# Performance work log

Measured on AMD Instinct MI355X. Metric: run time of the kernel, lower is better.

## Reference

```python
import jax, jax.numpy as jnp
import numpy as np

N_GROUPS = 4


def setup_inputs() -> dict:
    key = jax.random.key(0)
    ks = jax.random.split(key, 6)
    I, J, B = 512, 512, 4  # query tokens, key tokens, grid batch (B = 1 * n_groups)
    n_dim, out_per_group = 128, 4  # n_heads // n_groups = 16 // 4
    grid_q = jax.random.normal(ks[0], (I, 3), dtype=jnp.float32)
    grid_kv = jax.random.normal(ks[1], (B, J, 3), dtype=jnp.float32)
    W1 = jax.random.normal(ks[2], (3, n_dim), dtype=jnp.float32) * (1.0 / np.sqrt(3))
    b1 = jnp.zeros((n_dim,), dtype=jnp.float32)
    W2 = jax.random.normal(ks[3], (n_dim, n_dim), dtype=jnp.float32) * (1.0 / np.sqrt(n_dim))
    b2 = jnp.zeros((n_dim,), dtype=jnp.float32)
    W3 = jax.random.normal(ks[4], (n_dim, out_per_group), dtype=jnp.float32) * (1.0 / np.sqrt(n_dim))
    b3 = jnp.zeros((out_per_group,), dtype=jnp.float32)
    return {"grid_q": grid_q, "grid_kv": grid_kv, "W1": W1, "b1": b1,
            "W2": W2, "b2": b2, "W3": W3, "b3": b3}


def reference(grid_q, grid_kv, W1, b1, W2, b2, W3, b3):
    # grid_q: [I, 3] -> [1, I, 3]; grid_kv: [B, J, 3]
    gq = grid_q[None, :, :]
    # pairwise position difference: [B, I, J, 3]
    pos = gq[:, :, None, :] - grid_kv[:, None, :, :]
    # sign-log transform
    bias = jnp.sign(pos) * jnp.log1p(jnp.abs(pos))
    # tiny MLP: 3 -> n_dim -> n_dim -> heads//groups, pointwise over (B, I, J)
    h = jax.nn.relu(jnp.einsum('bijc,cd->bijd', bias, W1) + b1)
    h = jax.nn.relu(jnp.einsum('bijd,de->bije', h, W2) + b2)
    out = jnp.einsum('bije,eo->bijo', h, W3) + b3  # [B, I, J, O]
    # rearrange '(b g) i j o -> b (g o) i j' with g = N_GROUPS
    B, I, J, O = out.shape
    out = out.reshape(B // N_GROUPS, N_GROUPS, I, J, O)
    out = jnp.transpose(out, (0, 1, 4, 2, 3)).reshape(B // N_GROUPS, N_GROUPS * O, I, J)
    return out
```

## Files before the change

### kernel.cpp

```cpp
#include <hip/hip_runtime.h>
#include <math.h>

#define NDIM 128
#define TILE 64
#define NBLOCKS 2048
#define POS_PER_BLOCK 512
#define ITERS 8
#define CH 512

typedef __attribute__((ext_vector_type(8)))  short  short8;
typedef __attribute__((ext_vector_type(4)))  float  float4v;
typedef __attribute__((ext_vector_type(16))) float  float16;

__device__ __forceinline__ unsigned cvt_pk(float lo, float hi) {
    unsigned r;
    asm("v_cvt_pk_bf16_f32 %0, %1, %2" : "=v"(r) : "v"(lo), "v"(hi));
    return r;
}

__device__ __forceinline__ int kmap(int c, int jj) {
    return 32 * (c >> 2) + 16 * ((c >> 1) & 1) + 4 * (c & 1) + ((jj >> 2) << 3) + (jj & 3);
}

__global__ __launch_bounds__(256, 3)
void crpb_mfma4(const float* __restrict__ gq,
                const float* __restrict__ gkv,
                const float* __restrict__ W1,
                const float* __restrict__ b1,
                const float* __restrict__ W2,
                const float* __restrict__ b2,
                const float* __restrict__ W3,
                const float* __restrict__ b3,
                float* __restrict__ out)
{
    __shared__ __align__(16) unsigned short ash[16 * CH];
    __shared__ __align__(16) unsigned short h2s[16 * CH];
    __shared__ __align__(16) float b2s[NDIM];

    const int tid   = threadIdx.x;
    const int lane  = tid & 63;
    const int w     = __builtin_amdgcn_readfirstlane(tid >> 6);
    const int l31   = lane & 31;
    const int lhalf = lane >> 5;
    const int m16   = lane & 15;
    const int q16   = lane >> 4;

    if (tid < NDIM) b2s[tid] = b2[tid];

    const int ct = w;

    short8 a2f[8];
    #pragma unroll
    for (int ks = 0; ks < 8; ++ks) {
        const int c = 2 * ks + lhalf;
        unsigned t0[4];
        #pragma unroll
        for (int t = 0; t < 4; ++t) {
            const int d0 = kmap(c, 2 * t), d1 = d0 + 1;
            const int e0 = ct * 32 + l31;
            t0[t] = cvt_pk(W2[d0 * 128 + e0], W2[d1 * 128 + e0]);
        }
        __builtin_memcpy(&a2f[ks], t0, 16);
    }

    short8 w3t[4];
    #pragma unroll
    for (int ks = 0; ks < 4; ++ks) {
        const int c = ks * 4 + q16;
        unsigned tt[4];
        #pragma unroll
        for (int t = 0; t < 4; ++t) {
            const int k0 = kmap(c, 2 * t), k1 = k0 + 1;
            const float lo = (m16 < 4) ? W3[k0 * 4 + m16] : 0.0f;
            const float hi = (m16 < 4) ? W3[k1 * 4 + m16] : 0.0f;
            tt[t] = cvt_pk(lo, hi);
        }
        __builtin_memcpy(&w3t[ks], tt, 16);
    }
    float b3v[4];
    #pragma unroll
    for (int r = 0; r < 4; ++r) b3v[r] = (q16 == 0) ? b3[r] : 0.0f;

    __syncthreads();

    const int posblock = blockIdx.x * POS_PER_BLOCK;
    const int bb = posblock >> 18;
    const int i  = (posblock >> 9) & 511;
    const float q0 = gq[i * 3 + 0], q1 = gq[i * 3 + 1], q2 = gq[i * 3 + 2];

    unsigned short* aw        = ash + 4 * w * CH + lane * 8;
    const unsigned short* br  = ash + lhalf * CH + l31 * 8;
    unsigned short* cw        = h2s + (4 * ct + lhalf) * CH + l31 * 8;
    const unsigned short* dr  = h2s + q16 * CH + (w * 16 + m16) * 8;

    const float* kvp0 = gkv + (size_t)((bb << 9) + lane) * 3;
    float* obase = out + (((size_t)bb) << 20) + ((size_t)i << 9) + w * 16 + m16;

    float kv0 = kvp0[0], kv1 = kvp0[1], kv2 = kvp0[2];

    for (int it = 0; it < ITERS; ++it) {
        const int jb = it * TILE;

        {
            const float d0 = q0 - kv0, d1 = q1 - kv1, d2 = q2 - kv2;
            const float* kvn = kvp0 + ((it + 1) & 7) * (TILE * 3);
            kv0 = kvn[0]; kv1 = kvn[1]; kv2 = kvn[2];

            const float f0 = copysignf(__logf(1.0f + fabsf(d0)), d0);
            const float f1 = copysignf(__logf(1.0f + fabsf(d1)), d1);
            const float f2 = copysignf(__logf(1.0f + fabsf(d2)), d2);
            #pragma unroll
            for (int u = 0; u < 4; ++u) {
                const int c = 4 * w + u;
                unsigned pk[4];
                #pragma unroll
                for (int t = 0; t < 4; ++t) {
                    const int ch0 = kmap(c, 2 * t), ch1 = ch0 + 1;
                    float h0 = fmaf(f2, W1[256 + ch0], fmaf(f1, W1[128 + ch0],
                               fmaf(f0, W1[ch0], b1[ch0])));
                    float h1 = fmaf(f2, W1[256 + ch1], fmaf(f1, W1[128 + ch1],
                               fmaf(f0, W1[ch1], b1[ch1])));
                    pk[t] = cvt_pk(fmaxf(h0, 0.0f), fmaxf(h1, 0.0f));
                }
                short8 v; __builtin_memcpy(&v, pk, 16);
                *(short8*)(aw + u * CH) = v;
            }
        }
        __syncthreads();

        float16 acc0, acc1;
        #pragma unroll
        for (int qr = 0; qr < 4; ++qr) {
            float4v i0 = *(const float4v*)&b2s[ct * 32 + 8 * qr + 4 * lhalf];
            #pragma unroll
            for (int t = 0; t < 4; ++t) { acc0[4 * qr + t] = i0[t]; acc1[4 * qr + t] = i0[t]; }
        }
        #pragma unroll
        for (int ks = 0; ks < 8; ++ks) {
            short8 bf0 = *(const short8*)(br + ks * 2 * CH);
            short8 bf1 = *(const short8*)(br + ks * 2 * CH + 256);
            acc0 = __builtin_amdgcn_mfma_f32_32x32x16_bf16(a2f[ks], bf0, acc0, 0, 0, 0);
            acc1 = __builtin_amdgcn_mfma_f32_32x32x16_bf16(a2f[ks], bf1, acc1, 0, 0, 0);
        }

        {
            unsigned p0[4], p1[4], p2[4], p3[4];
            #pragma unroll
            for (int t = 0; t < 4; ++t) {
                p0[t] = cvt_pk(fmaxf(acc0[2 * t], 0.f),     fmaxf(acc0[2 * t + 1], 0.f));
                p1[t] = cvt_pk(fmaxf(acc0[8 + 2 * t], 0.f), fmaxf(acc0[8 + 2 * t + 1], 0.f));
                p2[t] = cvt_pk(fmaxf(acc1[2 * t], 0.f),     fmaxf(acc1[2 * t + 1], 0.f));
                p3[t] = cvt_pk(fmaxf(acc1[8 + 2 * t], 0.f), fmaxf(acc1[8 + 2 * t + 1], 0.f));
            }
            short8 v0, v1, v2, v3;
            __builtin_memcpy(&v0, p0, 16); __builtin_memcpy(&v1, p1, 16);
            __builtin_memcpy(&v2, p2, 16); __builtin_memcpy(&v3, p3, 16);
            *(short8*)(cw + 0 * CH) = v0;
            *(short8*)(cw + 2 * CH) = v1;
            *(short8*)(cw + 0 * CH + 256) = v2;
            *(short8*)(cw + 2 * CH + 256) = v3;
        }
        __syncthreads();

        {
            float4v acc3;
            #pragma unroll
            for (int r = 0; r < 4; ++r) acc3[r] = b3v[r];
            #pragma unroll
            for (int ks = 0; ks < 4; ++ks) {
                short8 bfrag = *(const short8*)(dr + ks * 4 * CH);
                acc3 = __builtin_amdgcn_mfma_f32_16x16x32_bf16(w3t[ks], bfrag, acc3, 0, 0, 0);
            }
            if (q16 == 0) {
                #pragma unroll
                for (int r = 0; r < 4; ++r)
                    obase[(size_t)(r << 18) + jb] = acc3[r];
            }
        }
    }
}

extern "C" void kernel_launch(void* const* d_in, const int* in_sizes, int n_in,
                              void* d_out, int out_size, void* d_ws, size_t ws_size,
                              hipStream_t stream) {
    const float* gq  = (const float*)d_in[0];
    const float* gkv = (const float*)d_in[1];
    const float* W1  = (const float*)d_in[2];
    const float* b1  = (const float*)d_in[3];
    const float* W2  = (const float*)d_in[4];
    const float* b2  = (const float*)d_in[5];
    const float* W3  = (const float*)d_in[6];
    const float* b3  = (const float*)d_in[7];
    float* out = (float*)d_out;

    crpb_mfma4<<<NBLOCKS, 256, 0, stream>>>(gq, gkv, W1, b1, W2, b2, W3, b3, out);
}
```

Measured before the change: 127.2 us.

## Double-buffer layer-1 tiles, split layer-3 across waves with LDS reduction

New measurement: 127.2 us. No clear change (+0.0%).

```diff
diff --git a/kernel.cpp b/kernel.cpp
--- a/kernel.cpp
+++ b/kernel.cpp
@@ -3,9 +3,10 @@
 
 #define NDIM 128
 #define TILE 64
-#define NBLOCKS 2048
-#define POS_PER_BLOCK 512
-#define ITERS 8
+#define NBLOCKS 1024
+#define THREADS 512
+#define POS_PER_BLOCK 1024
+#define ITERS 16
 #define CH 512
 
 typedef __attribute__((ext_vector_type(8)))  short  short8;
@@ -22,8 +23,8 @@
     return 32 * (c >> 2) + 16 * ((c >> 1) & 1) + 4 * (c & 1) + ((jj >> 2) << 3) + (jj & 3);
 }
 
-__global__ __launch_bounds__(256, 3)
-void crpb_mfma4(const float* __restrict__ gq,
+__global__ __launch_bounds__(512, 4)
+void crpb_mfma6(const float* __restrict__ gq,
                 const float* __restrict__ gkv,
                 const float* __restrict__ W1,
                 const float* __restrict__ b1,
@@ -33,26 +34,25 @@
                 const float* __restrict__ b3,
                 float* __restrict__ out)
 {
-    __shared__ __align__(16) unsigned short ash[16 * CH];
-    __shared__ __align__(16) unsigned short h2s[16 * CH];
+    __shared__ __align__(16) unsigned short ash[2][16 * CH];
+    __shared__ __align__(16) float red[2][4 * 4 * 64];
     __shared__ __align__(16) float b2s[NDIM];
 
-    const int tid   = threadIdx.x;
-    const int lane  = tid & 63;
-    const int w     = __builtin_amdgcn_readfirstlane(tid >> 6);
-    const int l31   = lane & 31;
-    const int lhalf = lane >> 5;
-    const int m16   = lane & 15;
-    const int q16   = lane >> 4;
+    const int tid  = threadIdx.x;
+    const int lane = tid & 63;
+    const int w    = __builtin_amdgcn_readfirstlane(tid >> 6);
+    const int l31  = lane & 31;
+    const int lh   = lane >> 5;
 
     if (tid < NDIM) b2s[tid] = b2[tid];
 
-    const int ct = w;
+    const int ct = w & 3;
+    const int ph = w >> 2;
 
     short8 a2f[8];
     #pragma unroll
     for (int ks = 0; ks < 8; ++ks) {
-        const int c = 2 * ks + lhalf;
+        const int c = 2 * ks + lh;
         unsigned t0[4];
         #pragma unroll
         for (int t = 0; t < 4; ++t) {
@@ -63,119 +63,114 @@
         __builtin_memcpy(&a2f[ks], t0, 16);
     }
 
-    short8 w3t[4];
+    short8 w3a[2];
     #pragma unroll
-    for (int ks = 0; ks < 4; ++ks) {
-        const int c = ks * 4 + q16;
+    for (int m = 0; m < 2; ++m) {
         unsigned tt[4];
         #pragma unroll
         for (int t = 0; t < 4; ++t) {
-            const int k0 = kmap(c, 2 * t), k1 = k0 + 1;
-            const float lo = (m16 < 4) ? W3[k0 * 4 + m16] : 0.0f;
-            const float hi = (m16 < 4) ? W3[k1 * 4 + m16] : 0.0f;
+            const int chl = ((2 * t) & 3) + 8 * ((2 * t) >> 2) + 4 * lh + 16 * m;
+            const int ch0 = ct * 32 + chl, ch1 = ch0 + 1;
+            const float lo = (l31 < 4) ? W3[ch0 * 4 + l31] : 0.0f;
+            const float hi = (l31 < 4) ? W3[ch1 * 4 + l31] : 0.0f;
             tt[t] = cvt_pk(lo, hi);
         }
-        __builtin_memcpy(&w3t[ks], tt, 16);
+        __builtin_memcpy(&w3a[m], tt, 16);
     }
-    float b3v[4];
-    #pragma unroll
-    for (int r = 0; r < 4; ++r) b3v[r] = (q16 == 0) ? b3[r] : 0.0f;
-
-    __syncthreads();
+    const float b3r = b3[(tid >> 6) & 3];
 
     const int posblock = blockIdx.x * POS_PER_BLOCK;
     const int bb = posblock >> 18;
-    const int i  = (posblock >> 9) & 511;
-    const float q0 = gq[i * 3 + 0], q1 = gq[i * 3 + 1], q2 = gq[i * 3 + 2];
+    const float* kvrow = gkv + (size_t)(bb << 9) * 3;
 
-    unsigned short* aw        = ash + 4 * w * CH + lane * 8;
-    const unsigned short* br  = ash + lhalf * CH + l31 * 8;
-    unsigned short* cw        = h2s + (4 * ct + lhalf) * CH + l31 * 8;
-    const unsigned short* dr  = h2s + q16 * CH + (w * 16 + m16) * 8;
+    int ii = (posblock >> 9) & 511;
+    float q0 = gq[ii * 3 + 0], q1 = gq[ii * 3 + 1], q2 = gq[ii * 3 + 2];
+    const float* kp = kvrow + (size_t)((posblock & 511) + lane) * 3;
+    float kv0 = kp[0], kv1 = kp[1], kv2 = kp[2];
 
-    const float* kvp0 = gkv + (size_t)((bb << 9) + lane) * 3;
-    float* obase = out + (((size_t)bb) << 20) + ((size_t)i << 9) + w * 16 + m16;
+    auto phaseA = [&](int x, int buf) {
+        const float c0 = q0 - kv0, c1 = q1 - kv1, c2 = q2 - kv2;
+        const int pn = posblock + (((x + 1) & 15) << 6);
+        const int iN = (pn >> 9) & 511, jN = pn & 511;
+        q0 = gq[iN * 3 + 0]; q1 = gq[iN * 3 + 1]; q2 = gq[iN * 3 + 2];
+        const float* kn = kvrow + (size_t)(jN + lane) * 3;
+        kv0 = kn[0]; kv1 = kn[1]; kv2 = kn[2];
 
-    float kv0 = kvp0[0], kv1 = kvp0[1], kv2 = kvp0[2];
+        const float f0 = copysignf(__logf(1.0f + fabsf(c0)), c0);
+        const float f1 = copysignf(__logf(1.0f + fabsf(c1)), c1);
+        const float f2 = copysignf(__logf(1.0f + fabsf(c2)), c2);
+        #pragma unroll
+        for (int u = 0; u < 2; ++u) {
+            const int c = 2 * w + u;
+            unsigned pk[4];
+            #pragma unroll
+            for (int t = 0; t < 4; ++t) {
+                const int ch0 = kmap(c, 2 * t), ch1 = ch0 + 1;
+                float h0 = fmaf(f2, W1[256 + ch0], fmaf(f1, W1[128 + ch0],
+                           fmaf(f0, W1[ch0], b1[ch0])));
+                float h1 = fmaf(f2, W1[256 + ch1], fmaf(f1, W1[128 + ch1],
+                           fmaf(f0, W1[ch1], b1[ch1])));
+                pk[t] = cvt_pk(fmaxf(h0, 0.0f), fmaxf(h1, 0.0f));
+            }
+            short8 v; __builtin_memcpy(&v, pk, 16);
+            *(short8*)&ash[buf][c * CH + lane * 8] = v;
+        }
+    };
+
+    phaseA(0, 0);
+    __syncthreads();
 
     for (int it = 0; it < ITERS; ++it) {
-        const int jb = it * TILE;
+        const int buf = it & 1;
+        const int posbase = posblock + it * TILE;
+        const int i  = (posbase >> 9) & 511;
+        const int jb = posbase & 511;
 
-        {
-            const float d0 = q0 - kv0, d1 = q1 - kv1, d2 = q2 - kv2;
-            const float* kvn = kvp0 + ((it + 1) & 7) * (TILE * 3);
-            kv0 = kvn[0]; kv1 = kvn[1]; kv2 = kvn[2];
-
-            const float f0 = copysignf(__logf(1.0f + fabsf(d0)), d0);
-            const float f1 = copysignf(__logf(1.0f + fabsf(d1)), d1);
-            const float f2 = copysignf(__logf(1.0f + fabsf(d2)), d2);
-            #pragma unroll
-            for (int u = 0; u < 4; ++u) {
-                const int c = 4 * w + u;
-                unsigned pk[4];
-                #pragma unroll
-                for (int t = 0; t < 4; ++t) {
-                    const int ch0 = kmap(c, 2 * t), ch1 = ch0 + 1;
-                    float h0 = fmaf(f2, W1[256 + ch0], fmaf(f1, W1[128 + ch0],
-                               fmaf(f0, W1[ch0], b1[ch0])));
-                    float h1 = fmaf(f2, W1[256 + ch1], fmaf(f1, W1[128 + ch1],
-                               fmaf(f0, W1[ch1], b1[ch1])));
-                    pk[t] = cvt_pk(fmaxf(h0, 0.0f), fmaxf(h1, 0.0f));
-                }
-                short8 v; __builtin_memcpy(&v, pk, 16);
-                *(short8*)(aw + u * CH) = v;
-            }
-        }
-        __syncthreads();
-
-        float16 acc0, acc1;
+        float16 acc;
         #pragma unroll
         for (int qr = 0; qr < 4; ++qr) {
-            float4v i0 = *(const float4v*)&b2s[ct * 32 + 8 * qr + 4 * lhalf];
+            float4v iv = *(const float4v*)&b2s[ct * 32 + 8 * qr + 4 * lh];
             #pragma unroll
-            for (int t = 0; t < 4; ++t) { acc0[4 * qr + t] = i0[t]; acc1[4 * qr + t] = i0[t]; }
+            for (int t = 0; t < 4; ++t) acc[4 * qr + t] = iv[t];
         }
+        const unsigned short* br = &ash[buf][lh * CH + (ph * 32 + l31) * 8];
         #pragma unroll
         for (int ks = 0; ks < 8; ++ks) {
-            short8 bf0 = *(const short8*)(br + ks * 2 * CH);
-            short8 bf1 = *(const short8*)(br + ks * 2 * CH + 256);
-            acc0 = __builtin_amdgcn_mfma_f32_32x32x16_bf16(a2f[ks], bf0, acc0, 0, 0, 0);
-            acc1 = __builtin_amdgcn_mfma_f32_32x32x16_bf16(a2f[ks], bf1, acc1, 0, 0, 0);
+            short8 bfrag = *(const short8*)(br + ks * 2 * CH);
+            acc = __builtin_amdgcn_mfma_f32_32x32x16_bf16(a2f[ks], bfrag, acc, 0, 0, 0);
         }
 
         {
-            unsigned p0[4], p1[4], p2[4], p3[4];
+            unsigned pk0[4], pk1[4];
             #pragma unroll
             for (int t = 0; t < 4; ++t) {
-                p0[t] = cvt_pk(fmaxf(acc0[2 * t], 0.f),     fmaxf(acc0[2 * t + 1], 0.f));
-                p1[t] = cvt_pk(fmaxf(acc0[8 + 2 * t], 0.f), fmaxf(acc0[8 + 2 * t + 1], 0.f));
-                p2[t] = cvt_pk(fmaxf(acc1[2 * t], 0.f),     fmaxf(acc1[2 * t + 1], 0.f));
-                p3[t] = cvt_pk(fmaxf(acc1[8 + 2 * t], 0.f), fmaxf(acc1[8 + 2 * t + 1], 0.f));
+                pk0[t] = cvt_pk(fmaxf(acc[2 * t], 0.f),     fmaxf(acc[2 * t + 1], 0.f));
+                pk1[t] = cvt_pk(fmaxf(acc[8 + 2 * t], 0.f), fmaxf(acc[8 + 2 * t + 1], 0.f));
             }
-            short8 v0, v1, v2, v3;
-            __builtin_memcpy(&v0, p0, 16); __builtin_memcpy(&v1, p1, 16);
-            __builtin_memcpy(&v2, p2, 16); __builtin_memcpy(&v3, p3, 16);
-            *(short8*)(cw + 0 * CH) = v0;
-            *(short8*)(cw + 2 * CH) = v1;
-            *(short8*)(cw + 0 * CH + 256) = v2;
-            *(short8*)(cw + 2 * CH + 256) = v3;
+            short8 bm0, bm1;
+            __builtin_memcpy(&bm0, pk0, 16);
+            __builtin_memcpy(&bm1, pk1, 16);
+            float16 p;
+            #pragma unroll
+            for (int r = 0; r < 16; ++r) p[r] = 0.0f;
+            p = __builtin_amdgcn_mfma_f32_32x32x16_bf16(w3a[0], bm0, p, 0, 0, 0);
+            p = __builtin_amdgcn_mfma_f32_32x32x16_bf16(w3a[1], bm1, p, 0, 0, 0);
+            if (lh == 0) {
+                #pragma unroll
+                for (int o = 0; o < 4; ++o)
+                    red[buf][(ct * 4 + o) * 64 + ph * 32 + l31] = p[o];
+            }
         }
+
+        if (it != ITERS - 1) phaseA(it + 1, 1 - buf);
+
         __syncthreads();
 
-        {
-            float4v acc3;
-            #pragma unroll
-            for (int r = 0; r < 4; ++r) acc3[r] = b3v[r];
-            #pragma unroll
-            for (int ks = 0; ks < 4; ++ks) {
-                short8 bfrag = *(const short8*)(dr + ks * 4 * CH);
-                acc3 = __builtin_amdgcn_mfma_f32_16x16x32_bf16(w3t[ks], bfrag, acc3, 0, 0, 0);
-            }
-            if (q16 == 0) {
-                #pragma unroll
-                for (int r = 0; r < 4; ++r)
-                    obase[(size_t)(r << 18) + jb] = acc3[r];
-            }
+        if (tid < 256) {
+            const int o = tid >> 6, pos = tid & 63;
+            const float* rb = &red[buf][o * 64 + pos];
+            const float v = b3r + rb[0] + rb[256] + rb[512] + rb[768];
+            out[((size_t)((bb << 2) + o) << 18) + ((size_t)i << 9) + jb + pos] = v;
         }
     }
 }
@@ -193,5 +188,5 @@
     const float* b3  = (const float*)d_in[7];
     float* out = (float*)d_out;
 
-    crpb_mfma4<<<NBLOCKS, 256, 0, stream>>>(gq, gkv, W1, b1, W2, b2, W3, b3, out);
+    crpb_mfma6<<<NBLOCKS, THREADS, 0, stream>>>(gq, gkv, W1, b1, W2, b2, W3, b3, out);
 }
```
